# Performance work log

Hardware: AMD Instinct MI355X
Metric: run time of the kernel (lower is better)

Reference implementation:

```python
import jax, jax.numpy as jnp
import numpy as np

N = 100_000   # nodes
E = 1_200_000 # edges
D = 64        # in_dim
H = 64        # hidden_dim
B = 1000      # graphs in batch
C = 10        # num_classes
TOPO = 64     # topo_dim
BN_EPS = 1e-5


def setup_inputs() -> dict:
    key = jax.random.key(0)
    ks = jax.random.split(key, 24)
    x = jax.random.normal(ks[0], (N, D), dtype=jnp.float32)
    edge_index = jax.random.randint(ks[1], (2, E), 0, N, dtype=jnp.int32)
    # sorted graph ids; force last id = B-1 so batch.max()+1 == B (matches torch path)
    batch = jnp.sort(jax.random.randint(ks[2], (N,), 0, B, dtype=jnp.int32)).at[-1].set(B - 1)
    topo = jax.random.normal(ks[3], (B, TOPO), dtype=jnp.float32)
    s = 0.05
    return {
        "x": x, "edge_index": edge_index, "batch": batch, "topo": topo,
        # conv1 MLP: Linear(D,H) -> BN(H) -> ReLU -> Linear(H,H) -> ReLU
        "W1a": jax.random.normal(ks[4], (D, H)) * s, "b1a": jax.random.normal(ks[5], (H,)) * s,
        "g1": 1.0 + jax.random.normal(ks[6], (H,)) * s, "be1": jax.random.normal(ks[7], (H,)) * s,
        "m1": jax.random.normal(ks[8], (H,)) * s, "v1": 0.5 + jax.random.uniform(ks[9], (H,)),
        "W1b": jax.random.normal(ks[10], (H, H)) * s, "b1b": jax.random.normal(ks[11], (H,)) * s,
        # conv2 MLP: Linear(H,H) -> BN(H) -> ReLU
        "W2": jax.random.normal(ks[12], (H, H)) * s, "b2": jax.random.normal(ks[13], (H,)) * s,
        "g2": 1.0 + jax.random.normal(ks[14], (H,)) * s, "be2": jax.random.normal(ks[15], (H,)) * s,
        "m2": jax.random.normal(ks[16], (H,)) * s, "v2": 0.5 + jax.random.uniform(ks[17], (H,)),
        # topo_net: Linear(TOPO,H) -> ReLU
        "Wt": jax.random.normal(ks[18], (TOPO, H)) * s, "bt": jax.random.normal(ks[19], (H,)) * s,
        # classifier: Linear(2H, C)
        "Wc": jax.random.normal(ks[20], (2 * H, C)) * s, "bc": jax.random.normal(ks[21], (C,)) * s,
    }


def _bn_eval(v, g, b, m, var):
    # BatchNorm1d in eval mode: affine with running stats
    return g * (v - m) * jax.lax.rsqrt(var + BN_EPS) + b


def _gin_agg(h, src, dst):
    # GINConv (eps=0): (1+eps)*x_i + sum_{j->i} x_j ; scatter-add over dst
    return h + jax.ops.segment_sum(h[src], dst, num_segments=N)


def reference(x, edge_index, batch, topo,
              W1a, b1a, g1, be1, m1, v1, W1b, b1b,
              W2, b2, g2, be2, m2, v2, Wt, bt, Wc, bc):
    src, dst = edge_index[0], edge_index[1]
    # conv1: MLP(agg(x)) = Lin -> BN -> ReLU -> Lin -> ReLU; outer relu from forward
    h = _gin_agg(x, src, dst)                              # [N, D]
    h = jax.nn.relu(_bn_eval(h @ W1a + b1a, g1, be1, m1, v1))
    h = jax.nn.relu(h @ W1b + b1b)                         # [N, H]
    h = jax.nn.relu(h)                                     # F.relu(conv1(...))
    # dropout(p=0.5) is identity in eval mode
    # conv2: Lin -> BN -> ReLU, then outer relu
    h = _gin_agg(h, src, dst)                              # [N, H]
    h = jax.nn.relu(_bn_eval(h @ W2 + b2, g2, be2, m2, v2))
    h = jax.nn.relu(h)
    # global_add_pool: sum nodes per graph
    x_struct = jax.ops.segment_sum(h, batch, num_segments=B)   # [B, H]
    # topo already [B, TOPO] => all reshape/pad branches are no-ops
    x_topo = jax.nn.relu(topo @ Wt + bt)                   # [B, H]
    combined = jnp.concatenate([x_struct, x_topo], axis=1) # [B, 2H]
    return combined @ Wc + bc                              # [B, C]
```

## Files before the change

kernel.cpp:

```cpp
#include <hip/hip_runtime.h>

#define N_NODES 100000
#define N_EDGES 1200000
#define DIM     64
#define BGRAPHS 1000
#define NCLASS  10
#define BN_EPS  1e-5f

#define NBUCK   256
#define NPB     391
#define MAGIC   10984572u
#define CHUNK   8192
#define NBLK_P  147
#define CAP     8192
#define NB_G    1563

typedef __attribute__((ext_vector_type(8))) short   bfx8;
typedef __attribute__((ext_vector_type(4))) float   f32x4;
typedef __attribute__((ext_vector_type(8))) unsigned short u16x8;

__device__ __forceinline__ unsigned short f2bf(float f) {
    unsigned u = __builtin_bit_cast(unsigned, f);
    unsigned r = (u + 0x7FFFu + ((u >> 16) & 1u)) >> 16;
    return (unsigned short)r;
}
__device__ __forceinline__ float bf2f(unsigned short h) {
    unsigned u = ((unsigned)h) << 16;
    return __builtin_bit_cast(float, u);
}

__device__ __forceinline__ bfx8 load_wfrag(const float* __restrict__ W, int kt, int q, int col) {
    bfx8 f;
    #pragma unroll
    for (int j = 0; j < 8; ++j)
        f[j] = (short)f2bf(W[(kt * 32 + q * 8 + j) * 64 + col]);
    return f;
}

__global__ __launch_bounds__(256) void prep_kernel(
    const float* __restrict__ x, const int* __restrict__ ei,
    int* __restrict__ gpart,
    const float* __restrict__ W1a, unsigned short* __restrict__ y0,
    float* __restrict__ xs,
    const float* __restrict__ W1b, const float* __restrict__ W2,
    unsigned short* __restrict__ w1bp, unsigned short* __restrict__ w2p,
    const float* __restrict__ b1a, const float* __restrict__ g1,
    const float* __restrict__ be1, const float* __restrict__ m1,
    const float* __restrict__ v1,
    const float* __restrict__ b2,  const float* __restrict__ g2,
    const float* __restrict__ be2, const float* __restrict__ m2,
    const float* __restrict__ v2,
    float* __restrict__ AB) {
    __shared__ int cnt[NBUCK];
    __shared__ unsigned short outt[4][16 * 64];
    int t = threadIdx.x;
    if (blockIdx.x < NBLK_P) {
        int blk = blockIdx.x;
        cnt[t] = 0;
        __syncthreads();
        int e0 = blk * CHUNK;
        for (int i = t; i < CHUNK; i += 256) {
            int e = e0 + i;
            if (e >= N_EDGES) break;
            unsigned d = (unsigned)ei[N_EDGES + e];
            atomicAdd(&cnt[__umulhi(d, MAGIC)], 1);
        }
        __syncthreads();
        gpart[blk * NBUCK + t] = cnt[t];
    } else if (blockIdx.x < NBLK_P + NB_G) {
        int g = blockIdx.x - NBLK_P;
        if (g < (BGRAPHS * DIM) / 256) xs[g * 256 + t] = 0.f;
        int w = t >> 6, lane = t & 63;
        int m = lane & 15, q = lane >> 4;
        int row0 = g * 64 + w * 16;

        bfx8 wa[4][2];
        #pragma unroll
        for (int nt = 0; nt < 4; ++nt)
            #pragma unroll
            for (int kt = 0; kt < 2; ++kt)
                wa[nt][kt] = load_wfrag(W1a, kt, q, nt * 16 + m);

        int rowA = row0 + m;
        if (rowA > N_NODES - 1) rowA = N_NODES - 1;
        const float* xp = x + (long long)rowA * 64;
        bfx8 a0, a1;
        #pragma unroll
        for (int j = 0; j < 8; ++j) {
            a0[j] = (short)f2bf(xp[q * 8 + j]);
            a1[j] = (short)f2bf(xp[32 + q * 8 + j]);
        }
        f32x4 acc[4];
        #pragma unroll
        for (int nt = 0; nt < 4; ++nt) {
            acc[nt] = (f32x4){0.f, 0.f, 0.f, 0.f};
            acc[nt] = __builtin_amdgcn_mfma_f32_16x16x32_bf16(a0, wa[nt][0], acc[nt], 0, 0, 0);
            acc[nt] = __builtin_amdgcn_mfma_f32_16x16x32_bf16(a1, wa[nt][1], acc[nt], 0, 0, 0);
        }
        #pragma unroll
        for (int nt = 0; nt < 4; ++nt)
            #pragma unroll
            for (int r = 0; r < 4; ++r)
                outt[w][(q * 4 + r) * 64 + nt * 16 + m] = f2bf(acc[nt][r]);
        __syncthreads();
        #pragma unroll
        for (int i = lane; i < 128; i += 64) {
            int rr = i >> 3, cc = i & 7;
            int rg = row0 + rr;
            if (rg < N_NODES)
                ((float4*)y0)[(long long)rg * 8 + cc] = *(const float4*)&outt[w][rr * 64 + cc * 8];
        }
    } else {
        const float* Ws[2] = {W1b, W2};
        unsigned short* Wp[2] = {w1bp, w2p};
        #pragma unroll
        for (int wsel = 0; wsel < 2; ++wsel) {
            const float* W = Ws[wsel];
            #pragma unroll
            for (int r = 0; r < 2; ++r) {
                int e = r * 256 + t;
                int kt = e >> 8, q = (e >> 6) & 3, col = e & 63;
                u16x8 o;
                #pragma unroll
                for (int j = 0; j < 8; ++j)
                    o[j] = f2bf(W[(kt * 32 + q * 8 + j) * 64 + col]);
                ((u16x8*)Wp[wsel])[e] = o;
            }
        }
        if (t < 64) {
            float s1 = g1[t] * rsqrtf(v1[t] + BN_EPS);
            AB[t]       = s1;
            AB[64 + t]  = b1a[t] * s1 + (be1[t] - m1[t] * s1);
            float s2 = g2[t] * rsqrtf(v2[t] + BN_EPS);
            AB[128 + t] = s2;
            AB[192 + t] = b2[t] * s2 + (be2[t] - m2[t] * s2);
        }
    }
}

__global__ __launch_bounds__(256) void scanB_kernel(const int* __restrict__ gpart,
                                                    int* __restrict__ base,
                                                    int* __restrict__ cursor) {
    __shared__ int tmp[256];
    int t = threadIdx.x;
    int s = 0;
    for (int blk = 0; blk < NBLK_P; ++blk) s += gpart[blk * NBUCK + t];
    tmp[t] = s;
    __syncthreads();
    for (int off = 1; off < 256; off <<= 1) {
        int a = (t >= off) ? tmp[t - off] : 0;
        __syncthreads();
        tmp[t] += a;
        __syncthreads();
    }
    int excl = tmp[t] - s;
    base[t] = excl;
    cursor[t] = excl;
    if (t == 255) base[256] = N_EDGES;
}

__global__ __launch_bounds__(256) void part_kernel(const int* __restrict__ ei,
                                                   const int* __restrict__ gpart,
                                                   int* __restrict__ cursor,
                                                   int* __restrict__ srcbuf,
                                                   unsigned short* __restrict__ dstlbuf) {
    __shared__ int cur[NBUCK];
    int t = threadIdx.x, blk = blockIdx.x;
    cur[t] = atomicAdd(&cursor[t], gpart[blk * NBUCK + t]);
    __syncthreads();
    int e0 = blk * CHUNK;
    for (int i = t; i < CHUNK; i += 256) {
        int e = e0 + i;
        if (e >= N_EDGES) break;
        unsigned d = (unsigned)ei[N_EDGES + e];
        int s = ei[e];
        int b = __umulhi(d, MAGIC);
        int pos = atomicAdd(&cur[b], 1);
        srcbuf[pos] = s;
        dstlbuf[pos] = (unsigned short)(d - b * NPB);
    }
}

__global__ __launch_bounds__(256) void refine_kernel(const int* __restrict__ srcbuf,
                                                     const unsigned short* __restrict__ dstlbuf,
                                                     const int* __restrict__ base,
                                                     int* __restrict__ csr_src,
                                                     int* __restrict__ rowptr) {
    __shared__ int cnt[NPB + 1];
    __shared__ int cur[NPB + 1];
    __shared__ int tmp[256];
    __shared__ int outb[CAP];
    int t = threadIdx.x, b = blockIdx.x;
    int beg = base[b];
    int end = base[b + 1];

    for (int i = t; i < NPB + 1; i += 256) cnt[i] = 0;
    __syncthreads();
    for (int i = beg + t; i < end; i += 256)
        atomicAdd(&cnt[dstlbuf[i]], 1);
    __syncthreads();

    int i0 = 2 * t, i1 = 2 * t + 1;
    int v0 = (i0 < NPB) ? cnt[i0] : 0;
    int v1 = (i1 < NPB) ? cnt[i1] : 0;
    int s = v0 + v1;
    tmp[t] = s;
    __syncthreads();
    for (int off = 1; off < 256; off <<= 1) {
        int a = (t >= off) ? tmp[t - off] : 0;
        __syncthreads();
        tmp[t] += a;
        __syncthreads();
    }
    int excl = tmp[t] - s;
    if (i0 < NPB) cur[i0] = excl;
    if (i1 < NPB) cur[i1] = excl + v0;
    {
        int g0 = b * NPB + i0;
        if (i0 < NPB && g0 < N_NODES) rowptr[g0] = beg + excl;
        int g1 = b * NPB + i1;
        if (i1 < NPB && g1 < N_NODES) rowptr[g1] = beg + excl + v0;
    }
    if (b == NBUCK - 1 && t == 0) rowptr[N_NODES] = N_EDGES;
    __syncthreads();

    for (int i = beg + t; i < end; i += 256) {
        int dl = dstlbuf[i];
        int pos = atomicAdd(&cur[dl], 1);
        if (pos < CAP) outb[pos] = srcbuf[i];
    }
    __syncthreads();

    int nb = end - beg; if (nb > CAP) nb = CAP;
    for (int i = t; i < nb; i += 256) csr_src[beg + i] = outb[i];
}

__global__ __launch_bounds__(256) void gather_bn1_kernel(
    const unsigned short* __restrict__ feat,
    const int* __restrict__ rowptr, const int* __restrict__ csr_src,
    const float* __restrict__ AB,
    unsigned short* __restrict__ out) {
    int t = threadIdx.x;
    int node = blockIdx.x * 32 + (t >> 3);
    int q = t & 7;
    const u16x8* f8 = (const u16x8*)feat;
    u16x8 sv = f8[(long long)node * 8 + q];
    float acc[8];
    #pragma unroll
    for (int j = 0; j < 8; ++j) acc[j] = bf2f(sv[j]);
    int beg = rowptr[node], end = rowptr[node + 1];
    int k = beg;
    int sn = (k < end) ? csr_src[k] : 0;
    while (k < end) {
        int sc = sn;
        ++k;
        if (k < end) sn = csr_src[k];
        u16x8 v = f8[(long long)sc * 8 + q];
        #pragma unroll
        for (int j = 0; j < 8; ++j) acc[j] += bf2f(v[j]);
    }
    u16x8 o;
    #pragma unroll
    for (int j = 0; j < 8; ++j) {
        int c = q * 8 + j;
        o[j] = f2bf(fmaxf(acc[j] * AB[c] + AB[64 + c], 0.f));
    }
    ((u16x8*)out)[(long long)node * 8 + q] = o;
}

__global__ __launch_bounds__(256) void mlpmid_kernel(
    const unsigned short* __restrict__ h1,
    const unsigned short* __restrict__ w1bp, const float* __restrict__ b1b,
    const unsigned short* __restrict__ w2p,
    unsigned short* __restrict__ y2) {
    __shared__ unsigned short h2t[4][16 * 72];
    __shared__ unsigned short outt[4][16 * 64];

    int t = threadIdx.x;
    int w = t >> 6, lane = t & 63;
    int m = lane & 15, q = lane >> 4;
    int row0 = blockIdx.x * 64 + w * 16;

    const bfx8* wbp = (const bfx8*)w1bp;
    const bfx8* wcp = (const bfx8*)w2p;
    bfx8 wb[4][2], wc[4][2];
    #pragma unroll
    for (int nt = 0; nt < 4; ++nt)
        #pragma unroll
        for (int kt = 0; kt < 2; ++kt) {
            int idx = (kt * 4 + q) * 64 + nt * 16 + m;
            wb[nt][kt] = wbp[idx];
            wc[nt][kt] = wcp[idx];
        }
    float B1b[4];
    #pragma unroll
    for (int nt = 0; nt < 4; ++nt) B1b[nt] = b1b[nt * 16 + m];

    int rowA = row0 + m;
    if (rowA > N_NODES - 1) rowA = N_NODES - 1;
    const bfx8* ap = (const bfx8*)(h1 + (long long)rowA * 64);
    bfx8 a0 = ap[q];
    bfx8 a1 = ap[4 + q];
    f32x4 acc[4];
    #pragma unroll
    for (int nt = 0; nt < 4; ++nt) {
        acc[nt] = (f32x4){0.f, 0.f, 0.f, 0.f};
        acc[nt] = __builtin_amdgcn_mfma_f32_16x16x32_bf16(a0, wb[nt][0], acc[nt], 0, 0, 0);
        acc[nt] = __builtin_amdgcn_mfma_f32_16x16x32_bf16(a1, wb[nt][1], acc[nt], 0, 0, 0);
    }
    #pragma unroll
    for (int nt = 0; nt < 4; ++nt)
        #pragma unroll
        for (int r = 0; r < 4; ++r) {
            float v = fmaxf(acc[nt][r] + B1b[nt], 0.f);
            h2t[w][(q * 4 + r) * 72 + nt * 16 + m] = f2bf(v);
        }
    __syncthreads();

    const bfx8* hp = (const bfx8*)&h2t[w][m * 72];
    bfx8 c0 = hp[q];
    bfx8 c1 = hp[4 + q];
    f32x4 acc2[4];
    #pragma unroll
    for (int nt = 0; nt < 4; ++nt) {
        acc2[nt] = (f32x4){0.f, 0.f, 0.f, 0.f};
        acc2[nt] = __builtin_amdgcn_mfma_f32_16x16x32_bf16(c0, wc[nt][0], acc2[nt], 0, 0, 0);
        acc2[nt] = __builtin_amdgcn_mfma_f32_16x16x32_bf16(c1, wc[nt][1], acc2[nt], 0, 0, 0);
    }
    #pragma unroll
    for (int nt = 0; nt < 4; ++nt)
        #pragma unroll
        for (int r = 0; r < 4; ++r)
            outt[w][(q * 4 + r) * 64 + nt * 16 + m] = f2bf(acc2[nt][r]);
    __syncthreads();

    #pragma unroll
    for (int i = lane; i < 128; i += 64) {
        int rr = i >> 3, cc = i & 7;
        int rg = row0 + rr;
        if (rg < N_NODES)
            ((float4*)y2)[(long long)rg * 8 + cc] = *(const float4*)&outt[w][rr * 64 + cc * 8];
    }
}

__global__ __launch_bounds__(256) void gather_pool_kernel(
    const unsigned short* __restrict__ feat,
    const int* __restrict__ rowptr, const int* __restrict__ csr_src,
    const float* __restrict__ AB, const int* __restrict__ batch,
    float* __restrict__ xs) {
    __shared__ float h4[32 * 65];
    __shared__ int bts[32];
    int t = threadIdx.x;
    int nl = t >> 3;
    int q = t & 7;
    int node = blockIdx.x * 32 + nl;
    if (t < 32) bts[t] = batch[blockIdx.x * 32 + t];
    const u16x8* f8 = (const u16x8*)feat;
    u16x8 sv = f8[(long long)node * 8 + q];
    float acc[8];
    #pragma unroll
    for (int j = 0; j < 8; ++j) acc[j] = bf2f(sv[j]);
    int beg = rowptr[node], end = rowptr[node + 1];
    int k = beg;
    int sn = (k < end) ? csr_src[k] : 0;
    while (k < end) {
        int sc = sn;
        ++k;
        if (k < end) sn = csr_src[k];
        u16x8 v = f8[(long long)sc * 8 + q];
        #pragma unroll
        for (int j = 0; j < 8; ++j) acc[j] += bf2f(v[j]);
    }
    #pragma unroll
    for (int j = 0; j < 8; ++j) {
        int c = q * 8 + j;
        h4[nl * 65 + c] = fmaxf(acc[j] * AB[128 + c] + AB[192 + c], 0.f);
    }
    __syncthreads();

    int col = t & 63;
    int r0 = (t >> 6) * 8;
    int cb = bts[r0];
    float cur = 0.f;
    #pragma unroll
    for (int r = 0; r < 8; ++r) {
        int b = bts[r0 + r];
        if (b != cb) {
            unsafeAtomicAdd(&xs[cb * 64 + col], cur);
            cb = b;
            cur = 0.f;
        }
        cur += h4[(r0 + r) * 65 + col];
    }
    unsafeAtomicAdd(&xs[cb * 64 + col], cur);
}

__global__ __launch_bounds__(64) void head_kernel(
    const float* __restrict__ xs, const float* __restrict__ topo,
    const float* __restrict__ Wt, const float* __restrict__ bt,
    const float* __restrict__ Wc, const float* __restrict__ bc,
    float* __restrict__ out) {
    __shared__ float trow[64];
    __shared__ float comb[128];
    int b = blockIdx.x;
    int h = threadIdx.x;
    trow[h] = topo[b * 64 + h];
    __syncthreads();
    float acc = bt[h];
    #pragma unroll
    for (int k = 0; k < 64; ++k) acc += trow[k] * Wt[k * 64 + h];
    comb[h] = xs[b * 64 + h];
    comb[64 + h] = fmaxf(acc, 0.f);
    __syncthreads();
    if (h < NCLASS) {
        float o = bc[h];
        #pragma unroll
        for (int k = 0; k < 128; ++k) o += comb[k] * Wc[k * NCLASS + h];
        out[b * NCLASS + h] = o;
    }
}

extern "C" void kernel_launch(void* const* d_in, const int* in_sizes, int n_in,
                              void* d_out, int out_size, void* d_ws, size_t ws_size,
                              hipStream_t stream) {
    const float* x     = (const float*)d_in[0];
    const int*   ei    = (const int*)d_in[1];
    const int*   batch = (const int*)d_in[2];
    const float* topo  = (const float*)d_in[3];
    const float* W1a   = (const float*)d_in[4];
    const float* b1a   = (const float*)d_in[5];
    const float* g1    = (const float*)d_in[6];
    const float* be1   = (const float*)d_in[7];
    const float* m1    = (const float*)d_in[8];
    const float* v1    = (const float*)d_in[9];
    const float* W1b   = (const float*)d_in[10];
    const float* b1b   = (const float*)d_in[11];
    const float* W2    = (const float*)d_in[12];
    const float* b2    = (const float*)d_in[13];
    const float* g2    = (const float*)d_in[14];
    const float* be2   = (const float*)d_in[15];
    const float* m2    = (const float*)d_in[16];
    const float* v2    = (const float*)d_in[17];
    const float* Wt    = (const float*)d_in[18];
    const float* bt    = (const float*)d_in[19];
    const float* Wc    = (const float*)d_in[20];
    const float* bc    = (const float*)d_in[21];
    float* out = (float*)d_out;

    char* p = (char*)d_ws;
    unsigned short* y0   = (unsigned short*)p; p += (size_t)N_NODES * DIM * 2;
    unsigned short* h1b  = (unsigned short*)p; p += (size_t)N_NODES * DIM * 2;
    unsigned short* y2b  = (unsigned short*)p; p += (size_t)N_NODES * DIM * 2;
    float* xs      = (float*)p; p += (size_t)BGRAPHS * DIM * 4;
    int*   rowptr  = (int*)p;   p += (size_t)(N_NODES + 16) * 4;
    int*   gpart   = (int*)p;   p += (size_t)NBLK_P * NBUCK * 4;
    int*   base    = (int*)p;   p += 1040;
    int*   cursor  = (int*)p;   p += 1024;
    unsigned short* w1bp = (unsigned short*)p; p += 512 * 16;
    unsigned short* w2p  = (unsigned short*)p; p += 512 * 16;
    float* AB      = (float*)p; p += 256 * 4;
    int*   srcbuf  = (int*)p;   p += (size_t)N_EDGES * 4;
    unsigned short* dstlbuf = (unsigned short*)p; p += (size_t)N_EDGES * 2;
    int*   csr_src = (int*)p;

    prep_kernel<<<NBLK_P + NB_G + 1, 256, 0, stream>>>(
        x, ei, gpart, W1a, y0, xs, W1b, W2, w1bp, w2p,
        b1a, g1, be1, m1, v1, b2, g2, be2, m2, v2, AB);
    scanB_kernel<<<1, 256, 0, stream>>>(gpart, base, cursor);
    part_kernel<<<NBLK_P, 256, 0, stream>>>(ei, gpart, cursor, srcbuf, dstlbuf);
    refine_kernel<<<NBUCK, 256, 0, stream>>>(srcbuf, dstlbuf, base, csr_src, rowptr);
    gather_bn1_kernel<<<N_NODES / 32, 256, 0, stream>>>(y0, rowptr, csr_src, AB, h1b);
    mlpmid_kernel<<<(N_NODES + 63) / 64, 256, 0, stream>>>(h1b, w1bp, b1b, w2p, y2b);
    gather_pool_kernel<<<N_NODES / 32, 256, 0, stream>>>(y2b, rowptr, csr_src, AB, batch, xs);
    head_kernel<<<BGRAPHS, 64, 0, stream>>>(xs, topo, Wt, bt, Wc, bc, out);
}
```

Measured before the change: 238.3 us.

## Fuse first gather with MLP matmuls and fold bucket scan into partition

The neighbor gather plus BN1/ReLU is merged with the two MFMA linear layers into one kernel, so the intermediate h1 no longer makes a round trip through global memory and one launch goes away. The single-block scan kernel is removed. Every partition block now recomputes the bucket prefix sum redundantly and adds it to a zero-based cursor that prep_kernel resets. This saves a launch and a serial dependency, at the cost of repeated gpart reads in each of the 147 blocks and a split of MFMA work across waves with weights reloaded per block.

```diff
diff --git a/kernel.cpp b/kernel.cpp
--- a/kernel.cpp
+++ b/kernel.cpp
@@ -50,7 +50,7 @@
     const float* __restrict__ b2,  const float* __restrict__ g2,
     const float* __restrict__ be2, const float* __restrict__ m2,
     const float* __restrict__ v2,
-    float* __restrict__ AB) {
+    float* __restrict__ AB, int* __restrict__ cursor) {
     __shared__ int cnt[NBUCK];
     __shared__ unsigned short outt[4][16 * 64];
     int t = threadIdx.x;
@@ -111,6 +111,7 @@
                 ((float4*)y0)[(long long)rg * 8 + cc] = *(const float4*)&outt[w][rr * 64 + cc * 8];
         }
     } else {
+        cursor[t] = 0;
         const float* Ws[2] = {W1b, W2};
         unsigned short* Wp[2] = {w1bp, w2p};
         #pragma unroll
@@ -138,45 +139,40 @@
     }
 }
 
-__global__ __launch_bounds__(256) void scanB_kernel(const int* __restrict__ gpart,
-                                                    int* __restrict__ base,
-                                                    int* __restrict__ cursor) {
-    __shared__ int tmp[256];
-    int t = threadIdx.x;
-    int s = 0;
-    for (int blk = 0; blk < NBLK_P; ++blk) s += gpart[blk * NBUCK + t];
-    tmp[t] = s;
-    __syncthreads();
-    for (int off = 1; off < 256; off <<= 1) {
-        int a = (t >= off) ? tmp[t - off] : 0;
-        __syncthreads();
-        tmp[t] += a;
-        __syncthreads();
-    }
-    int excl = tmp[t] - s;
-    base[t] = excl;
-    cursor[t] = excl;
-    if (t == 255) base[256] = N_EDGES;
-}
-
 __global__ __launch_bounds__(256) void part_kernel(const int* __restrict__ ei,
                                                    const int* __restrict__ gpart,
                                                    int* __restrict__ cursor,
+                                                   int* __restrict__ base,
                                                    int* __restrict__ srcbuf,
                                                    unsigned short* __restrict__ dstlbuf) {
+    __shared__ int tmp[256];
     __shared__ int cur[NBUCK];
     int t = threadIdx.x, blk = blockIdx.x;
-    cur[t] = atomicAdd(&cursor[t], gpart[blk * NBUCK + t]);
+    int s = 0;
+    for (int b = 0; b < NBLK_P; ++b) s += gpart[b * NBUCK + t];
+    tmp[t] = s;
+    __syncthreads();
+    for (int off = 1; off < 256; off <<= 1) {
+        int a = (t >= off) ? tmp[t - off] : 0;
+        __syncthreads();
+        tmp[t] += a;
+        __syncthreads();
+    }
+    int excl = tmp[t] - s;
+    base[t] = excl;
+    if (blk == 0 && t == 255) base[256] = N_EDGES;
+    int resv = atomicAdd(&cursor[t], gpart[blk * NBUCK + t]);
+    cur[t] = excl + resv;
     __syncthreads();
     int e0 = blk * CHUNK;
     for (int i = t; i < CHUNK; i += 256) {
         int e = e0 + i;
         if (e >= N_EDGES) break;
         unsigned d = (unsigned)ei[N_EDGES + e];
-        int s = ei[e];
+        int sv = ei[e];
         int b = __umulhi(d, MAGIC);
         int pos = atomicAdd(&cur[b], 1);
-        srcbuf[pos] = s;
+        srcbuf[pos] = sv;
         dstlbuf[pos] = (unsigned short)(d - b * NPB);
     }
 }
@@ -235,112 +231,95 @@
     for (int i = t; i < nb; i += 256) csr_src[beg + i] = outb[i];
 }
 
-__global__ __launch_bounds__(256) void gather_bn1_kernel(
+__global__ __launch_bounds__(256) void gather_mlp1_kernel(
     const unsigned short* __restrict__ feat,
     const int* __restrict__ rowptr, const int* __restrict__ csr_src,
     const float* __restrict__ AB,
-    unsigned short* __restrict__ out) {
-    int t = threadIdx.x;
-    int node = blockIdx.x * 32 + (t >> 3);
-    int q = t & 7;
-    const u16x8* f8 = (const u16x8*)feat;
-    u16x8 sv = f8[(long long)node * 8 + q];
-    float acc[8];
-    #pragma unroll
-    for (int j = 0; j < 8; ++j) acc[j] = bf2f(sv[j]);
-    int beg = rowptr[node], end = rowptr[node + 1];
-    int k = beg;
-    int sn = (k < end) ? csr_src[k] : 0;
-    while (k < end) {
-        int sc = sn;
-        ++k;
-        if (k < end) sn = csr_src[k];
-        u16x8 v = f8[(long long)sc * 8 + q];
-        #pragma unroll
-        for (int j = 0; j < 8; ++j) acc[j] += bf2f(v[j]);
-    }
-    u16x8 o;
-    #pragma unroll
-    for (int j = 0; j < 8; ++j) {
-        int c = q * 8 + j;
-        o[j] = f2bf(fmaxf(acc[j] * AB[c] + AB[64 + c], 0.f));
-    }
-    ((u16x8*)out)[(long long)node * 8 + q] = o;
-}
-
-__global__ __launch_bounds__(256) void mlpmid_kernel(
-    const unsigned short* __restrict__ h1,
     const unsigned short* __restrict__ w1bp, const float* __restrict__ b1b,
     const unsigned short* __restrict__ w2p,
     unsigned short* __restrict__ y2) {
-    __shared__ unsigned short h2t[4][16 * 72];
-    __shared__ unsigned short outt[4][16 * 64];
+    __shared__ unsigned short h1t[32 * 72];
+    __shared__ unsigned short h2t[32 * 72];
+    __shared__ unsigned short outt[32 * 64];
 
     int t = threadIdx.x;
+    int nl = t >> 3, q8 = t & 7;
+    int node = blockIdx.x * 32 + nl;
+    const u16x8* f8 = (const u16x8*)feat;
+    {
+        u16x8 sv = f8[(long long)node * 8 + q8];
+        float acc[8];
+        #pragma unroll
+        for (int j = 0; j < 8; ++j) acc[j] = bf2f(sv[j]);
+        int beg = rowptr[node], end = rowptr[node + 1];
+        int k = beg;
+        int sn = (k < end) ? csr_src[k] : 0;
+        while (k < end) {
+            int sc = sn;
+            ++k;
+            if (k < end) sn = csr_src[k];
+            u16x8 v = f8[(long long)sc * 8 + q8];
+            #pragma unroll
+            for (int j = 0; j < 8; ++j) acc[j] += bf2f(v[j]);
+        }
+        #pragma unroll
+        for (int j = 0; j < 8; ++j) {
+            int c = q8 * 8 + j;
+            h1t[nl * 72 + c] = f2bf(fmaxf(acc[j] * AB[c] + AB[64 + c], 0.f));
+        }
+    }
+    __syncthreads();
+
     int w = t >> 6, lane = t & 63;
     int m = lane & 15, q = lane >> 4;
-    int row0 = blockIdx.x * 64 + w * 16;
+    int rt = w >> 1;
+    int c0 = (w & 1) * 2;
 
     const bfx8* wbp = (const bfx8*)w1bp;
     const bfx8* wcp = (const bfx8*)w2p;
-    bfx8 wb[4][2], wc[4][2];
-    #pragma unroll
-    for (int nt = 0; nt < 4; ++nt)
-        #pragma unroll
-        for (int kt = 0; kt < 2; ++kt) {
-            int idx = (kt * 4 + q) * 64 + nt * 16 + m;
-            wb[nt][kt] = wbp[idx];
-            wc[nt][kt] = wcp[idx];
-        }
-    float B1b[4];
-    #pragma unroll
-    for (int nt = 0; nt < 4; ++nt) B1b[nt] = b1b[nt * 16 + m];
-
-    int rowA = row0 + m;
-    if (rowA > N_NODES - 1) rowA = N_NODES - 1;
-    const bfx8* ap = (const bfx8*)(h1 + (long long)rowA * 64);
-    bfx8 a0 = ap[q];
-    bfx8 a1 = ap[4 + q];
-    f32x4 acc[4];
-    #pragma unroll
-    for (int nt = 0; nt < 4; ++nt) {
-        acc[nt] = (f32x4){0.f, 0.f, 0.f, 0.f};
-        acc[nt] = __builtin_amdgcn_mfma_f32_16x16x32_bf16(a0, wb[nt][0], acc[nt], 0, 0, 0);
-        acc[nt] = __builtin_amdgcn_mfma_f32_16x16x32_bf16(a1, wb[nt][1], acc[nt], 0, 0, 0);
-    }
-    #pragma unroll
-    for (int nt = 0; nt < 4; ++nt)
-        #pragma unroll
-        for (int r = 0; r < 4; ++r) {
-            float v = fmaxf(acc[nt][r] + B1b[nt], 0.f);
-            h2t[w][(q * 4 + r) * 72 + nt * 16 + m] = f2bf(v);
-        }
-    __syncthreads();
-
-    const bfx8* hp = (const bfx8*)&h2t[w][m * 72];
-    bfx8 c0 = hp[q];
-    bfx8 c1 = hp[4 + q];
-    f32x4 acc2[4];
-    #pragma unroll
-    for (int nt = 0; nt < 4; ++nt) {
-        acc2[nt] = (f32x4){0.f, 0.f, 0.f, 0.f};
-        acc2[nt] = __builtin_amdgcn_mfma_f32_16x16x32_bf16(c0, wc[nt][0], acc2[nt], 0, 0, 0);
-        acc2[nt] = __builtin_amdgcn_mfma_f32_16x16x32_bf16(c1, wc[nt][1], acc2[nt], 0, 0, 0);
-    }
-    #pragma unroll
-    for (int nt = 0; nt < 4; ++nt)
-        #pragma unroll
-        for (int r = 0; r < 4; ++r)
-            outt[w][(q * 4 + r) * 64 + nt * 16 + m] = f2bf(acc2[nt][r]);
-    __syncthreads();
-
-    #pragma unroll
-    for (int i = lane; i < 128; i += 64) {
-        int rr = i >> 3, cc = i & 7;
-        int rg = row0 + rr;
-        if (rg < N_NODES)
-            ((float4*)y2)[(long long)rg * 8 + cc] = *(const float4*)&outt[w][rr * 64 + cc * 8];
-    }
+
+    {
+        const bfx8* hp = (const bfx8*)&h1t[(rt * 16 + m) * 72];
+        bfx8 a0 = hp[q];
+        bfx8 a1 = hp[4 + q];
+        #pragma unroll
+        for (int ci = 0; ci < 2; ++ci) {
+            int ct = c0 + ci;
+            bfx8 w0 = wbp[(0 * 4 + q) * 64 + ct * 16 + m];
+            bfx8 w1 = wbp[(1 * 4 + q) * 64 + ct * 16 + m];
+            f32x4 acc = (f32x4){0.f, 0.f, 0.f, 0.f};
+            acc = __builtin_amdgcn_mfma_f32_16x16x32_bf16(a0, w0, acc, 0, 0, 0);
+            acc = __builtin_amdgcn_mfma_f32_16x16x32_bf16(a1, w1, acc, 0, 0, 0);
+            float bb = b1b[ct * 16 + m];
+            #pragma unroll
+            for (int r = 0; r < 4; ++r)
+                h2t[(rt * 16 + q * 4 + r) * 72 + ct * 16 + m] = f2bf(fmaxf(acc[r] + bb, 0.f));
+        }
+    }
+    __syncthreads();
+
+    {
+        const bfx8* hp = (const bfx8*)&h2t[(rt * 16 + m) * 72];
+        bfx8 a0 = hp[q];
+        bfx8 a1 = hp[4 + q];
+        #pragma unroll
+        for (int ci = 0; ci < 2; ++ci) {
+            int ct = c0 + ci;
+            bfx8 w0 = wcp[(0 * 4 + q) * 64 + ct * 16 + m];
+            bfx8 w1 = wcp[(1 * 4 + q) * 64 + ct * 16 + m];
+            f32x4 acc = (f32x4){0.f, 0.f, 0.f, 0.f};
+            acc = __builtin_amdgcn_mfma_f32_16x16x32_bf16(a0, w0, acc, 0, 0, 0);
+            acc = __builtin_amdgcn_mfma_f32_16x16x32_bf16(a1, w1, acc, 0, 0, 0);
+            #pragma unroll
+            for (int r = 0; r < 4; ++r)
+                outt[(rt * 16 + q * 4 + r) * 64 + ct * 16 + m] = f2bf(acc[r]);
+        }
+    }
+    __syncthreads();
+
+    int rr = t >> 3, cc = t & 7;
+    ((float4*)y2)[((long long)blockIdx.x * 32 + rr) * 8 + cc] =
+        *(const float4*)&outt[rr * 64 + cc * 8];
 }
 
 __global__ __launch_bounds__(256) void gather_pool_kernel(
@@ -449,7 +428,6 @@
 
     char* p = (char*)d_ws;
     unsigned short* y0   = (unsigned short*)p; p += (size_t)N_NODES * DIM * 2;
-    unsigned short* h1b  = (unsigned short*)p; p += (size_t)N_NODES * DIM * 2;
     unsigned short* y2b  = (unsigned short*)p; p += (size_t)N_NODES * DIM * 2;
     float* xs      = (float*)p; p += (size_t)BGRAPHS * DIM * 4;
     int*   rowptr  = (int*)p;   p += (size_t)(N_NODES + 16) * 4;
@@ -465,12 +443,11 @@
 
     prep_kernel<<<NBLK_P + NB_G + 1, 256, 0, stream>>>(
         x, ei, gpart, W1a, y0, xs, W1b, W2, w1bp, w2p,
-        b1a, g1, be1, m1, v1, b2, g2, be2, m2, v2, AB);
-    scanB_kernel<<<1, 256, 0, stream>>>(gpart, base, cursor);
-    part_kernel<<<NBLK_P, 256, 0, stream>>>(ei, gpart, cursor, srcbuf, dstlbuf);
+        b1a, g1, be1, m1, v1, b2, g2, be2, m2, v2, AB, cursor);
+    part_kernel<<<NBLK_P, 256, 0, stream>>>(ei, gpart, cursor, base, srcbuf, dstlbuf);
     refine_kernel<<<NBUCK, 256, 0, stream>>>(srcbuf, dstlbuf, base, csr_src, rowptr);
-    gather_bn1_kernel<<<N_NODES / 32, 256, 0, stream>>>(y0, rowptr, csr_src, AB, h1b);
-    mlpmid_kernel<<<(N_NODES + 63) / 64, 256, 0, stream>>>(h1b, w1bp, b1b, w2p, y2b);
+    gather_mlp1_kernel<<<N_NODES / 32, 256, 0, stream>>>(
+        y0, rowptr, csr_src, AB, w1bp, b1b, w2p, y2b);
     gather_pool_kernel<<<N_NODES / 32, 256, 0, stream>>>(y2b, rowptr, csr_src, AB, batch, xs);
     head_kernel<<<BGRAPHS, 64, 0, stream>>>(xs, topo, Wt, bt, Wc, bc, out);
 }
```

After: 228.9 us. 1.04x faster.
